# Optimization experiments

Hardware: AMD Instinct MI355X
Metric: run time of the kernel (lower is better)

The kernel has to match this reference:

```python
import jax, jax.numpy as jnp
import numpy as np

# ---- fixed problem dimensions ----
B, S, T = 64, 200, 32          # batch of sequences, trees per seq, nodes per tree
V, E, C = 50000, 128, 128      # vocab, embedding_dim, encode_dim
H, OUT = 100, 104              # GRU hidden, output_dim
N = B * S * T                  # total nodes
D_MAX = 5                      # max depth of a 32-node complete binary tree


def setup_inputs() -> dict:
    key = jax.random.key(0)
    ks = jax.random.split(key, 16)
    # --- tree structure: every tree is a complete binary tree with T nodes ---
    local_parent = np.array([0] + [(i - 1) // 2 for i in range(1, T)], dtype=np.int64)
    local_depth = np.array([int(np.floor(np.log2(i + 1))) for i in range(T)], dtype=np.int64)
    num_trees = B * S
    offsets = np.arange(num_trees, dtype=np.int64) * T
    node_parent = (offsets[:, None] + local_parent[None, :]).reshape(-1)
    node_depth = np.tile(local_depth, num_trees)
    node_tree = np.repeat(np.arange(num_trees, dtype=np.int64), T)
    node_tokens = jax.random.randint(ks[0], (N,), 0, V, dtype=jnp.int64)
    sc = 0.05
    inp = {
        "node_tokens": node_tokens,
        "node_parent": jnp.asarray(node_parent),
        "node_tree": jnp.asarray(node_tree),
        "node_depth": jnp.asarray(node_depth),
        "emb": jax.random.normal(ks[1], (V, E), jnp.float32) * sc,
        "w_lin": jax.random.normal(ks[2], (C, E), jnp.float32) * sc,
        "b_lin": jnp.zeros((C,), jnp.float32),
        "w_ih_f": jax.random.normal(ks[3], (3 * H, C), jnp.float32) * sc,
        "w_hh_f": jax.random.normal(ks[4], (3 * H, H), jnp.float32) * sc,
        "b_ih_f": jnp.zeros((3 * H,), jnp.float32),
        "b_hh_f": jnp.zeros((3 * H,), jnp.float32),
        "w_ih_b": jax.random.normal(ks[5], (3 * H, C), jnp.float32) * sc,
        "w_hh_b": jax.random.normal(ks[6], (3 * H, H), jnp.float32) * sc,
        "b_ih_b": jnp.zeros((3 * H,), jnp.float32),
        "b_hh_b": jnp.zeros((3 * H,), jnp.float32),
        "fc_w": jax.random.normal(ks[7], (OUT, 2 * H), jnp.float32) * sc,
        "fc_b": jnp.zeros((OUT,), jnp.float32),
    }
    return inp


def _gru(x_sbc, w_ih, w_hh, b_ih, b_hh):
    """Torch-convention GRU over leading time axis. x_sbc: [S, B, C] -> [S, B, H]."""
    h0 = jnp.zeros((x_sbc.shape[1], w_hh.shape[1]), x_sbc.dtype)

    def step(h, xt):
        gx = xt @ w_ih.T + b_ih
        gh = h @ w_hh.T + b_hh
        xr, xz, xn = jnp.split(gx, 3, axis=-1)
        hr, hz, hn = jnp.split(gh, 3, axis=-1)
        r = jax.nn.sigmoid(xr + hr)
        z = jax.nn.sigmoid(xz + hz)
        n = jnp.tanh(xn + r * hn)
        h_new = (1.0 - z) * n + z * h
        return h_new, h_new

    _, hs = jax.lax.scan(step, h0, x_sbc)
    return hs


def reference(node_tokens, node_parent, node_tree, node_depth,
              emb, w_lin, b_lin,
              w_ih_f, w_hh_f, b_ih_f, b_hh_f,
              w_ih_b, w_hh_b, b_ih_b, b_hh_b,
              fc_w, fc_b):
    # per-node contribution: W * emb(token) + b   (recursion base of hidden_state)
    c = emb[node_tokens] @ w_lin.T + b_lin               # [N, C]
    # level-batched bottom-up scatter-add: h(node) = c(node) + sum(h(children))
    h = c
    for d in range(D_MAX, 0, -1):
        mask = (node_depth == d)[:, None]
        h = h.at[node_parent].add(jnp.where(mask, h, 0.0))
    # per-tree max pool over all node hidden states (TreeEncoder output)
    tree_vec = jax.ops.segment_max(h, node_tree, num_segments=B * S)  # [B*S, C]
    x = tree_vec.reshape(B, S, C)
    # bidirectional GRU (batch_first in torch; scan over time here)
    x_t = jnp.transpose(x, (1, 0, 2))                    # [S, B, C]
    fwd = _gru(x_t, w_ih_f, w_hh_f, b_ih_f, b_hh_f)      # [S, B, H]
    bwd = _gru(x_t[::-1], w_ih_b, w_hh_b, b_ih_b, b_hh_b)[::-1]
    gru_out = jnp.concatenate([fwd, bwd], axis=-1)       # [S, B, 2H]
    pool = gru_out.max(axis=0)                           # [B, 2H] (max over time)
    return pool @ fc_w.T + fc_b                          # [B, OUT]
```

## Files before the change

kernel.cpp:

```cpp
#include <hip/hip_runtime.h>
#include <hip/hip_bf16.h>
#include <math.h>

#define BB 64
#define SS 200
#define TT 32
#define VV 50000
#define EE 128
#define CC 128
#define HH 100
#define G3 300
#define OUTD 104
#define NTREE (BB*SS)

typedef __attribute__((ext_vector_type(4))) float f32x4;
typedef _Float16 f16x8 __attribute__((ext_vector_type(8)));

#define L2E  1.4426950408889634f
#define NL2E (-1.4426950408889634f)
#define TL2E 2.8853900817779268f

#define BAR() asm volatile("s_waitcnt lgkmcnt(0)\n\ts_barrier" ::: "memory")


__global__ __launch_bounds__(256) void k0_prep(const float* __restrict__ w_lin,
                                               const float* __restrict__ w_ih_f,
                                               const float* __restrict__ w_ih_b,
                                               const float* __restrict__ emb,
                                               _Float16* __restrict__ wl,
                                               _Float16* __restrict__ k2b,
                                               _Float16* __restrict__ emb16) {
    const int tid  = threadIdx.x;
    const int wave = tid >> 6;
    const int lane = tid & 63;
    const int r = lane & 15;
    const int q = lane >> 4;
    if (blockIdx.x == 0) {
#pragma unroll
        for (int nt = 0; nt < 2; ++nt)
#pragma unroll
            for (int kt = 0; kt < 4; ++kt) {
                const int n = wave * 32 + nt * 16 + r;
                const float* src = w_lin + (long)n * EE + kt * 32 + q * 8;
                f16x8 f;
#pragma unroll
                for (int e = 0; e < 8; ++e) f[e] = (_Float16)src[e];
                *(f16x8*)&wl[(size_t)((((wave * 2 + nt) * 4 + kt) * 64) + lane) * 8] = f;
            }
    } else if (blockIdx.x <= 10) {
        const int nb = blockIdx.x - 1;
        const int n = nb * 64 + wave * 16 + r;
        const int dir = (n >= 320) ? 1 : 0;
        const int j = n - dir * 320;
        const int jj = (j < G3) ? j : 0;
        const float* w = dir ? w_ih_b : w_ih_f;
#pragma unroll
        for (int kt = 0; kt < 4; ++kt) {
            const float* src = w + (long)jj * EE + kt * 32 + q * 8;
            f16x8 f;
#pragma unroll
            for (int e = 0; e < 8; ++e) f[e] = (_Float16)src[e];
            *(f16x8*)&k2b[(size_t)((((nb * 4 + wave) * 4 + kt) * 64) + lane) * 8] = f;
        }
    } else {
        const long base = (long)(blockIdx.x - 11) * 2048 + (long)tid * 8;
        if (base < (long)VV * EE) {
            const float4* s = (const float4*)(emb + base);
            const float4 v0 = s[0], v1 = s[1];
            f16x8 f;
            f[0] = (_Float16)v0.x; f[1] = (_Float16)v0.y;
            f[2] = (_Float16)v0.z; f[3] = (_Float16)v0.w;
            f[4] = (_Float16)v1.x; f[5] = (_Float16)v1.y;
            f[6] = (_Float16)v1.z; f[7] = (_Float16)v1.w;
            *(f16x8*)&emb16[base] = f;
        }
    }
}

#define K1_TPI 2
#define AROWS (K1_TPI*TT)
#define LDA 136
#define LDC 132

__global__ __launch_bounds__(256) void k1_mfma(const int* __restrict__ tok,
                                               const _Float16* __restrict__ emb16,
                                               const _Float16* __restrict__ wl,
                                               const float* __restrict__ b_lin,
                                               _Float16* __restrict__ thi) {
    __shared__ __align__(16) _Float16 A_sh[AROWS * LDA];
    __shared__ __align__(16) float C_sh[AROWS * LDC];
    __shared__ int tok_sh[AROWS];

    const int tid  = threadIdx.x;
    const int wave = tid >> 6;
    const int lane = tid & 63;
    const int r = lane & 15;
    const int q = lane >> 4;

    f16x8 bfrag[2][4];
    float bias[2];
#pragma unroll
    for (int nt = 0; nt < 2; ++nt) {
        bias[nt] = b_lin[wave * 32 + nt * 16 + r];
#pragma unroll
        for (int kt = 0; kt < 4; ++kt)
            bfrag[nt][kt] = *(const f16x8*)&wl[(size_t)((((wave * 2 + nt) * 4 + kt) * 64) + lane) * 8];
    }

    const int tree0 = blockIdx.x * K1_TPI;
    if (tid < AROWS) tok_sh[tid] = tok[tree0 * TT + tid];
    __syncthreads();

#pragma unroll
    for (int i = 0; i < 4; ++i) {
        const int idx = tid + i * 256;
        const int row = idx >> 4;
        const int p   = idx & 15;
        const f16x8 v = *(const f16x8*)&emb16[(long)tok_sh[row] * EE + p * 8];
        *(f16x8*)&A_sh[row * LDA + p * 8] = v;
    }
    __syncthreads();

    f32x4 acc[4][2];
#pragma unroll
    for (int mt = 0; mt < 4; ++mt)
#pragma unroll
        for (int nt = 0; nt < 2; ++nt) acc[mt][nt] = (f32x4)(0.f);

#pragma unroll
    for (int mt = 0; mt < 4; ++mt) {
        const int m = mt * 16 + r;
        f16x8 afrag[4];
#pragma unroll
        for (int kt = 0; kt < 4; ++kt)
            afrag[kt] = *(const f16x8*)&A_sh[m * LDA + kt * 32 + q * 8];
#pragma unroll
        for (int nt = 0; nt < 2; ++nt)
#pragma unroll
            for (int kt = 0; kt < 4; ++kt)
                acc[mt][nt] = __builtin_amdgcn_mfma_f32_16x16x32_f16(
                    afrag[kt], bfrag[nt][kt], acc[mt][nt], 0, 0, 0);
    }

#pragma unroll
    for (int mt = 0; mt < 4; ++mt)
#pragma unroll
        for (int nt = 0; nt < 2; ++nt) {
            const int col = wave * 32 + nt * 16 + r;
#pragma unroll
            for (int reg = 0; reg < 4; ++reg) {
                const int row = mt * 16 + q * 4 + reg;
                C_sh[row * LDC + col] = acc[mt][nt][reg] + bias[nt];
            }
        }
    __syncthreads();

    {
        const int t = tid >> 7;
        const int j = tid & 127;
        const float* base = &C_sh[(t * TT) * LDC + j];
        float v[TT];
#pragma unroll
        for (int n = 0; n < TT; ++n) v[n] = base[n * LDC];
        float mx = -1e30f;
#pragma unroll
        for (int n = TT - 1; n >= 1; --n) {
            mx = fmaxf(mx, v[n]);
            v[(n - 1) >> 1] += v[n];
        }
        mx = fmaxf(mx, v[0]);
        thi[(size_t)(tree0 + t) * CC + j] = (_Float16)mx;
    }
}

__global__ __launch_bounds__(256) void k2_mfma(const _Float16* __restrict__ thi,
                                               const _Float16* __restrict__ k2b,
                                               const float* __restrict__ b_ih_f,
                                               const float* __restrict__ b_ih_b,
                                               const float* __restrict__ b_hh_f,
                                               const float* __restrict__ b_hh_b,
                                               float* __restrict__ gx) {
    __shared__ __align__(16) _Float16 Ah[32 * LDA];

    const int tid  = threadIdx.x;
    const int wave = tid >> 6;
    const int lane = tid & 63;
    const int r = lane & 15;
    const int q = lane >> 4;

    const int nb = blockIdx.x % 10;
    const int mb = blockIdx.x / 10;
    const int m0 = mb * 32;
    const int n0 = nb * 64;

#pragma unroll
    for (int i = 0; i < 2; ++i) {
        const int idx = tid + i * 256;
        const int row = idx >> 4;
        const int p   = idx & 15;
        f16x8 v = *(const f16x8*)&thi[(size_t)(m0 + row) * CC + p * 8];
        *(f16x8*)&Ah[row * LDA + p * 8] = v;
    }
    f16x8 bh[4];
#pragma unroll
    for (int kt = 0; kt < 4; ++kt)
        bh[kt] = *(const f16x8*)&k2b[(size_t)((((nb * 4 + wave) * 4 + kt) * 64) + lane) * 8];
    __syncthreads();

    f32x4 acc[2];
    acc[0] = (f32x4)(0.f); acc[1] = (f32x4)(0.f);
#pragma unroll
    for (int mt = 0; mt < 2; ++mt) {
        const int m = mt * 16 + r;
#pragma unroll
        for (int kt = 0; kt < 4; ++kt) {
            f16x8 a = *(const f16x8*)&Ah[m * LDA + kt * 32 + q * 8];
            acc[mt] = __builtin_amdgcn_mfma_f32_16x16x32_f16(a, bh[kt], acc[mt], 0, 0, 0);
        }
    }

    const int ng  = n0 + wave * 16 + r;
    const int dir = (ng >= 320) ? 1 : 0;
    const int j   = ng - dir * 320;
    const bool valid = (j < G3);
    const float* b_ih = dir ? b_ih_b : b_ih_f;
    const float* b_hh = dir ? b_hh_b : b_hh_f;
    const float bias = valid ? b_ih[j] : 0.f;
    const float bh2  = (valid && j < 2 * HH) ? b_hh[j] : 0.f;
    const float sc   = (j < 2 * HH) ? NL2E : TL2E;
    float* gxd = gx + (long)dir * NTREE * G3;
    if (valid) {
#pragma unroll
        for (int mt = 0; mt < 2; ++mt)
#pragma unroll
            for (int reg = 0; reg < 4; ++reg) {
                const int m = m0 + mt * 16 + q * 4 + reg;
                gxd[(long)m * G3 + j] = sc * (acc[mt][reg] + bias + bh2);
            }
    }
}

__global__ __launch_bounds__(256, 1) void k3_gru(const float* __restrict__ gx,
                                                 const float* __restrict__ w_hh_f,
                                                 const float* __restrict__ b_hh_f,
                                                 const float* __restrict__ w_hh_b,
                                                 const float* __restrict__ b_hh_b,
                                                 float* __restrict__ pool) {
    const int bid = blockIdx.x;
    const int dir = bid & 1;
    const int b = bid >> 1;
    const float* w_hh = dir ? w_hh_b : w_hh_f;
    const float* b_hh = dir ? b_hh_b : b_hh_f;

    __shared__ __align__(16) _Float16 h_sh[2][128];

    const int tid  = threadIdx.x;
    const int wave = tid >> 6;
    const int lane = tid & 63;
    const int r = lane & 15;
    const int q = lane >> 4;

    f16x8 bf[5][4];
#pragma unroll
    for (int i = 0; i < 5; ++i) {
        const int l = i * 16 + r;
        const int gate = l / 25;
        const int ch   = l - gate * 25;
        const bool nv  = (l < 75);
        const int row  = gate * HH + wave * 25 + ch;
        const float sc = (gate == 2) ? TL2E : NL2E;
#pragma unroll
        for (int kt = 0; kt < 4; ++kt) {
            f16x8 f;
#pragma unroll
            for (int e = 0; e < 8; ++e) {
                const int k = kt * 32 + q * 8 + e;
                f[e] = (_Float16)((nv && k < HH) ? sc * w_hh[row * HH + k] : 0.f);
            }
            bf[i][kt] = f;
        }
    }

    const int m = lane;
    const int c = wave * 25 + m;
    const bool act = (m < 25);
    const float bnc = act ? TL2E * b_hh[2 * HH + c] : 0.f;

    const int a_z  = (25 + m) & 63;
    const int a_n1 = (50 + m) & 63;
    const int a_n2 = (50 + m - 64) & 63;
    const bool nV1 = (50 + m) < 64;

    if (tid < 128) { h_sh[0][tid] = (_Float16)0.f; h_sh[1][tid] = (_Float16)0.f; }

    const int sstep = dir ? -1 : 1;
    const int s0 = dir ? (SS - 1) : 0;
    const float* gp = gx + (long)dir * NTREE * G3 + (long)b * SS * G3 + c;

    float pxr[4], pxz[4], pxn[4];
    if (act) {
#pragma unroll
        for (int j = 0; j < 4; ++j) {
            const long off = (long)(s0 + j * sstep) * G3;
            pxr[j] = gp[off]; pxz[j] = gp[off + HH]; pxn[j] = gp[off + 2 * HH];
        }
    }
    float hj = 0.f, hmax = -1e30f;
    __syncthreads();

    int s = s0;
    for (int t = 0; t < SS; t += 4) {
#pragma unroll
        for (int j = 0; j < 4; ++j) {
            const int p = j & 1;

            f16x8 a[4];
#pragma unroll
            for (int kt = 0; kt < 4; ++kt)
                a[kt] = *(const f16x8*)&h_sh[p][kt * 32 + q * 8];

            f32x4 accA[5], accB[5];
#pragma unroll
            for (int i = 0; i < 5; ++i) {
                accA[i] = (f32x4)(0.f);
                accB[i] = (f32x4)(0.f);
                accA[i] = __builtin_amdgcn_mfma_f32_16x16x32_f16(a[0], bf[i][0], accA[i], 0, 0, 0);
                accB[i] = __builtin_amdgcn_mfma_f32_16x16x32_f16(a[2], bf[i][2], accB[i], 0, 0, 0);
                accA[i] = __builtin_amdgcn_mfma_f32_16x16x32_f16(a[1], bf[i][1], accA[i], 0, 0, 0);
                accB[i] = __builtin_amdgcn_mfma_f32_16x16x32_f16(a[3], bf[i][3], accB[i], 0, 0, 0);
            }
            const float g0 = accA[0][0] + accB[0][0];
            const float g1 = accA[1][0] + accB[1][0];
            const float g2 = accA[2][0] + accB[2][0];
            const float g3 = accA[3][0] + accB[3][0];
            const float g4 = accA[4][0] + accB[4][0];
            float V1 = g0;
            V1 = (q == 1) ? g1 : V1;
            V1 = (q == 2) ? g2 : V1;
            V1 = (q == 3) ? g3 : V1;
            const float ghr = V1;
            const float ghz = __shfl(V1, a_z);
            const float vnA = __shfl(V1, a_n1);
            const float vnB = __shfl(g4, a_n2);
            const float ghn = nV1 ? vnA : vnB;

            if (act) {
                const float rg = __builtin_amdgcn_rcpf(1.f + __builtin_amdgcn_exp2f(pxr[j] + ghr));
                const float zg = __builtin_amdgcn_rcpf(1.f + __builtin_amdgcn_exp2f(pxz[j] + ghz));
                const float t1 = ghn + bnc;
                const float an = __builtin_fmaf(rg, t1, pxn[j]);
                const float u  = __builtin_amdgcn_rcpf(1.f + __builtin_amdgcn_exp2f(an));
                const float n  = __builtin_fmaf(-2.f, u, 1.f);
                hj = __builtin_fmaf(zg, hj - n, n);
                h_sh[1 - p][c] = (_Float16)hj;
                hmax = fmaxf(hmax, hj);
                if (t + j + 4 < SS) {
                    const long off = (long)(s + (j + 4) * sstep) * G3;
                    pxr[j] = gp[off]; pxz[j] = gp[off + HH]; pxn[j] = gp[off + 2 * HH];
                }
            }
            BAR();
        }
        s += 4 * sstep;
    }
    if (act) pool[(long)b * (2 * HH) + dir * HH + c] = hmax;
}

__global__ __launch_bounds__(256) void k4_fc(const float* __restrict__ pool,
                                             const float* __restrict__ fc_w,
                                             const float* __restrict__ fc_b,
                                             float* __restrict__ out) {
    const int b = blockIdx.x;
    __shared__ __align__(16) float p_sh[2 * HH];
    const int t = threadIdx.x;
    if (t < 2 * HH) p_sh[t] = pool[(long)b * (2 * HH) + t];
    __syncthreads();
    if (t < OUTD) {
        const float4* wr4 = (const float4*)(fc_w + (long)t * (2 * HH));
        const float4* p4 = (const float4*)p_sh;
        float a0 = 0.f, a1 = 0.f;
#pragma unroll
        for (int k = 0; k < 50; k += 2) {
            float4 w0 = wr4[k],   p0 = p4[k];
            float4 w1 = wr4[k+1], p1 = p4[k+1];
            a0 += w0.x*p0.x + w0.y*p0.y + w0.z*p0.z + w0.w*p0.w;
            a1 += w1.x*p1.x + w1.y*p1.y + w1.z*p1.z + w1.w*p1.w;
        }
        out[(long)b * OUTD + t] = fc_b[t] + a0 + a1;
    }
}

extern "C" void kernel_launch(void* const* d_in, const int* in_sizes, int n_in,
                              void* d_out, int out_size, void* d_ws, size_t ws_size,
                              hipStream_t stream) {
    const int*   tok    = (const int*)d_in[0];
    const float* emb    = (const float*)d_in[4];
    const float* w_lin  = (const float*)d_in[5];
    const float* b_lin  = (const float*)d_in[6];
    const float* w_ih_f = (const float*)d_in[7];
    const float* w_hh_f = (const float*)d_in[8];
    const float* b_ih_f = (const float*)d_in[9];
    const float* b_hh_f = (const float*)d_in[10];
    const float* w_ih_b = (const float*)d_in[11];
    const float* w_hh_b = (const float*)d_in[12];
    const float* b_ih_b = (const float*)d_in[13];
    const float* b_hh_b = (const float*)d_in[14];
    const float* fc_w   = (const float*)d_in[15];
    const float* fc_b   = (const float*)d_in[16];

    char* wsb = (char*)d_ws;
    _Float16* wl    = (_Float16*)(wsb);
    _Float16* k2b   = (_Float16*)(wsb + 32768);
    _Float16* thi   = (_Float16*)(wsb + 196608);
    float*    gx    = (float*)(wsb + 3473408);
    _Float16* emb16 = (_Float16*)(wsb + 3473408);
    float*    pool  = (float*)(wsb);
    float*    out   = (float*)d_out;

    k0_prep<<<11 + 3125, 256, 0, stream>>>(w_lin, w_ih_f, w_ih_b, emb, wl, k2b, emb16);
    k1_mfma<<<NTREE / K1_TPI, 256, 0, stream>>>(tok, emb16, wl, b_lin, thi);
    k2_mfma<<<(NTREE / 32) * 10, 256, 0, stream>>>(thi, k2b, b_ih_f, b_ih_b,
                                                   b_hh_f, b_hh_b, gx);
    k3_gru <<<2 * BB, 256, 0, stream>>>(gx, w_hh_f, b_hh_f, w_hh_b, b_hh_b, pool);
    k4_fc  <<<BB, 256, 0, stream>>>(pool, fc_w, fc_b, out);
}
```

Baseline: 232.0 us.

## Fuse embedding GEMM, tree reduce, and input-gate GEMM into one kernel

Drops the full fp32-to-fp16 conversion of the 50000x128 embedding table and instead gathers only the needed fp32 rows, converting them in-kernel. Merges the per-tree linear/tree-reduce kernel with the GRU input projection kernel, so each block processes 16 trees and keeps the pooled tree vectors in shared memory rather than round-tripping them through global memory. This removes a large conversion pass and one launch. In exchange, fp32 gathers double the bytes per gathered row, the grid has fewer, longer blocks with a serial loop, and there are extra barriers per chunk.

```diff
diff --git a/kernel.cpp b/kernel.cpp
--- a/kernel.cpp
+++ b/kernel.cpp
@@ -26,10 +26,8 @@
 __global__ __launch_bounds__(256) void k0_prep(const float* __restrict__ w_lin,
                                                const float* __restrict__ w_ih_f,
                                                const float* __restrict__ w_ih_b,
-                                               const float* __restrict__ emb,
                                                _Float16* __restrict__ wl,
-                                               _Float16* __restrict__ k2b,
-                                               _Float16* __restrict__ emb16) {
+                                               _Float16* __restrict__ k2b) {
     const int tid  = threadIdx.x;
     const int wave = tid >> 6;
     const int lane = tid & 63;
@@ -47,7 +45,7 @@
                 for (int e = 0; e < 8; ++e) f[e] = (_Float16)src[e];
                 *(f16x8*)&wl[(size_t)((((wave * 2 + nt) * 4 + kt) * 64) + lane) * 8] = f;
             }
-    } else if (blockIdx.x <= 10) {
+    } else {
         const int nb = blockIdx.x - 1;
         const int n = nb * 64 + wave * 16 + r;
         const int dir = (n >= 320) ? 1 : 0;
@@ -62,33 +60,28 @@
             for (int e = 0; e < 8; ++e) f[e] = (_Float16)src[e];
             *(f16x8*)&k2b[(size_t)((((nb * 4 + wave) * 4 + kt) * 64) + lane) * 8] = f;
         }
-    } else {
-        const long base = (long)(blockIdx.x - 11) * 2048 + (long)tid * 8;
-        if (base < (long)VV * EE) {
-            const float4* s = (const float4*)(emb + base);
-            const float4 v0 = s[0], v1 = s[1];
-            f16x8 f;
-            f[0] = (_Float16)v0.x; f[1] = (_Float16)v0.y;
-            f[2] = (_Float16)v0.z; f[3] = (_Float16)v0.w;
-            f[4] = (_Float16)v1.x; f[5] = (_Float16)v1.y;
-            f[6] = (_Float16)v1.z; f[7] = (_Float16)v1.w;
-            *(f16x8*)&emb16[base] = f;
-        }
-    }
-}
-
-#define K1_TPI 2
-#define AROWS (K1_TPI*TT)
+    }
+}
+
+#define TPB 16
+#define AROWS 64
 #define LDA 136
 #define LDC 132
 
-__global__ __launch_bounds__(256) void k1_mfma(const int* __restrict__ tok,
-                                               const _Float16* __restrict__ emb16,
-                                               const _Float16* __restrict__ wl,
-                                               const float* __restrict__ b_lin,
-                                               _Float16* __restrict__ thi) {
-    __shared__ __align__(16) _Float16 A_sh[AROWS * LDA];
-    __shared__ __align__(16) float C_sh[AROWS * LDC];
+__global__ __launch_bounds__(256, 4) void k12_fused(const int* __restrict__ tok,
+                                                    const float* __restrict__ emb,
+                                                    const _Float16* __restrict__ wl,
+                                                    const float* __restrict__ b_lin,
+                                                    const _Float16* __restrict__ k2b,
+                                                    const float* __restrict__ b_ih_f,
+                                                    const float* __restrict__ b_ih_b,
+                                                    const float* __restrict__ b_hh_f,
+                                                    const float* __restrict__ b_hh_b,
+                                                    float* __restrict__ gx) {
+    __shared__ __align__(16) char U_sh[AROWS * LDC * 4];
+    _Float16* A_sh = (_Float16*)U_sh;
+    float*    C_sh = (float*)U_sh;
+    __shared__ __align__(16) _Float16 thi_sh[TPB][LDA];
     __shared__ int tok_sh[AROWS];
 
     const int tid  = threadIdx.x;
@@ -97,6 +90,8 @@
     const int r = lane & 15;
     const int q = lane >> 4;
 
+    const int T0 = blockIdx.x * TPB;
+
     f16x8 bfrag[2][4];
     float bias[2];
 #pragma unroll
@@ -107,136 +102,109 @@
             bfrag[nt][kt] = *(const f16x8*)&wl[(size_t)((((wave * 2 + nt) * 4 + kt) * 64) + lane) * 8];
     }
 
-    const int tree0 = blockIdx.x * K1_TPI;
-    if (tid < AROWS) tok_sh[tid] = tok[tree0 * TT + tid];
+    for (int c = 0; c < 8; ++c) {
+        if (tid < AROWS) tok_sh[tid] = tok[(T0 + 2 * c) * TT + tid];
+        __syncthreads();
+
+#pragma unroll
+        for (int i = 0; i < 8; ++i) {
+            const int idx = tid + i * 256;
+            const int row = idx >> 5;
+            const int p   = idx & 31;
+            const float4 e = ((const float4*)(emb + (long)tok_sh[row] * EE))[p];
+            _Float16* dst = &A_sh[row * LDA + p * 4];
+            dst[0] = (_Float16)e.x; dst[1] = (_Float16)e.y;
+            dst[2] = (_Float16)e.z; dst[3] = (_Float16)e.w;
+        }
+        __syncthreads();
+
+        f32x4 acc[4][2];
+#pragma unroll
+        for (int mt = 0; mt < 4; ++mt)
+#pragma unroll
+            for (int nt = 0; nt < 2; ++nt) acc[mt][nt] = (f32x4)(0.f);
+
+#pragma unroll
+        for (int mt = 0; mt < 4; ++mt) {
+            const int m = mt * 16 + r;
+            f16x8 afrag[4];
+#pragma unroll
+            for (int kt = 0; kt < 4; ++kt)
+                afrag[kt] = *(const f16x8*)&A_sh[m * LDA + kt * 32 + q * 8];
+#pragma unroll
+            for (int nt = 0; nt < 2; ++nt)
+#pragma unroll
+                for (int kt = 0; kt < 4; ++kt)
+                    acc[mt][nt] = __builtin_amdgcn_mfma_f32_16x16x32_f16(
+                        afrag[kt], bfrag[nt][kt], acc[mt][nt], 0, 0, 0);
+        }
+        __syncthreads();
+
+#pragma unroll
+        for (int mt = 0; mt < 4; ++mt)
+#pragma unroll
+            for (int nt = 0; nt < 2; ++nt) {
+                const int col = wave * 32 + nt * 16 + r;
+#pragma unroll
+                for (int reg = 0; reg < 4; ++reg) {
+                    const int row = mt * 16 + q * 4 + reg;
+                    C_sh[row * LDC + col] = acc[mt][nt][reg] + bias[nt];
+                }
+            }
+        __syncthreads();
+
+        {
+            const int t = tid >> 7;
+            const int j = tid & 127;
+            const float* base = &C_sh[(t * TT) * LDC + j];
+            float v[TT];
+#pragma unroll
+            for (int n = 0; n < TT; ++n) v[n] = base[n * LDC];
+            float mx = -1e30f;
+#pragma unroll
+            for (int n = TT - 1; n >= 1; --n) {
+                mx = fmaxf(mx, v[n]);
+                v[(n - 1) >> 1] += v[n];
+            }
+            mx = fmaxf(mx, v[0]);
+            thi_sh[2 * c + t][j] = (_Float16)mx;
+        }
+    }
     __syncthreads();
 
-#pragma unroll
-    for (int i = 0; i < 4; ++i) {
-        const int idx = tid + i * 256;
-        const int row = idx >> 4;
-        const int p   = idx & 15;
-        const f16x8 v = *(const f16x8*)&emb16[(long)tok_sh[row] * EE + p * 8];
-        *(f16x8*)&A_sh[row * LDA + p * 8] = v;
-    }
-    __syncthreads();
-
-    f32x4 acc[4][2];
-#pragma unroll
-    for (int mt = 0; mt < 4; ++mt)
-#pragma unroll
-        for (int nt = 0; nt < 2; ++nt) acc[mt][nt] = (f32x4)(0.f);
-
-#pragma unroll
-    for (int mt = 0; mt < 4; ++mt) {
-        const int m = mt * 16 + r;
-        f16x8 afrag[4];
+    f16x8 a4[4];
+#pragma unroll
+    for (int kt = 0; kt < 4; ++kt)
+        a4[kt] = *(const f16x8*)&thi_sh[r][kt * 32 + q * 8];
+
+#pragma unroll
+    for (int nb = 0; nb < 10; ++nb) {
+        f16x8 bh[4];
 #pragma unroll
         for (int kt = 0; kt < 4; ++kt)
-            afrag[kt] = *(const f16x8*)&A_sh[m * LDA + kt * 32 + q * 8];
-#pragma unroll
-        for (int nt = 0; nt < 2; ++nt)
-#pragma unroll
-            for (int kt = 0; kt < 4; ++kt)
-                acc[mt][nt] = __builtin_amdgcn_mfma_f32_16x16x32_f16(
-                    afrag[kt], bfrag[nt][kt], acc[mt][nt], 0, 0, 0);
-    }
-
-#pragma unroll
-    for (int mt = 0; mt < 4; ++mt)
-#pragma unroll
-        for (int nt = 0; nt < 2; ++nt) {
-            const int col = wave * 32 + nt * 16 + r;
+            bh[kt] = *(const f16x8*)&k2b[(size_t)((((nb * 4 + wave) * 4 + kt) * 64) + lane) * 8];
+        f32x4 acc = (f32x4)(0.f);
+#pragma unroll
+        for (int kt = 0; kt < 4; ++kt)
+            acc = __builtin_amdgcn_mfma_f32_16x16x32_f16(a4[kt], bh[kt], acc, 0, 0, 0);
+
+        const int ng  = nb * 64 + wave * 16 + r;
+        const int dir = (ng >= 320) ? 1 : 0;
+        const int j   = ng - dir * 320;
+        const bool valid = (j < G3);
+        const float* b_ih = dir ? b_ih_b : b_ih_f;
+        const float* b_hh = dir ? b_hh_b : b_hh_f;
+        const float bias2 = valid ? b_ih[j] : 0.f;
+        const float bh2   = (valid && j < 2 * HH) ? b_hh[j] : 0.f;
+        const float sc    = (j < 2 * HH) ? NL2E : TL2E;
+        float* gxd = gx + (long)dir * NTREE * G3;
+        if (valid) {
 #pragma unroll
             for (int reg = 0; reg < 4; ++reg) {
-                const int row = mt * 16 + q * 4 + reg;
-                C_sh[row * LDC + col] = acc[mt][nt][reg] + bias[nt];
-            }
-        }
-    __syncthreads();
-
-    {
-        const int t = tid >> 7;
-        const int j = tid & 127;
-        const float* base = &C_sh[(t * TT) * LDC + j];
-        float v[TT];
-#pragma unroll
-        for (int n = 0; n < TT; ++n) v[n] = base[n * LDC];
-        float mx = -1e30f;
-#pragma unroll
-        for (int n = TT - 1; n >= 1; --n) {
-            mx = fmaxf(mx, v[n]);
-            v[(n - 1) >> 1] += v[n];
-        }
-        mx = fmaxf(mx, v[0]);
-        thi[(size_t)(tree0 + t) * CC + j] = (_Float16)mx;
-    }
-}
-
-__global__ __launch_bounds__(256) void k2_mfma(const _Float16* __restrict__ thi,
-                                               const _Float16* __restrict__ k2b,
-                                               const float* __restrict__ b_ih_f,
-                                               const float* __restrict__ b_ih_b,
-                                               const float* __restrict__ b_hh_f,
-                                               const float* __restrict__ b_hh_b,
-                                               float* __restrict__ gx) {
-    __shared__ __align__(16) _Float16 Ah[32 * LDA];
-
-    const int tid  = threadIdx.x;
-    const int wave = tid >> 6;
-    const int lane = tid & 63;
-    const int r = lane & 15;
-    const int q = lane >> 4;
-
-    const int nb = blockIdx.x % 10;
-    const int mb = blockIdx.x / 10;
-    const int m0 = mb * 32;
-    const int n0 = nb * 64;
-
-#pragma unroll
-    for (int i = 0; i < 2; ++i) {
-        const int idx = tid + i * 256;
-        const int row = idx >> 4;
-        const int p   = idx & 15;
-        f16x8 v = *(const f16x8*)&thi[(size_t)(m0 + row) * CC + p * 8];
-        *(f16x8*)&Ah[row * LDA + p * 8] = v;
-    }
-    f16x8 bh[4];
-#pragma unroll
-    for (int kt = 0; kt < 4; ++kt)
-        bh[kt] = *(const f16x8*)&k2b[(size_t)((((nb * 4 + wave) * 4 + kt) * 64) + lane) * 8];
-    __syncthreads();
-
-    f32x4 acc[2];
-    acc[0] = (f32x4)(0.f); acc[1] = (f32x4)(0.f);
-#pragma unroll
-    for (int mt = 0; mt < 2; ++mt) {
-        const int m = mt * 16 + r;
-#pragma unroll
-        for (int kt = 0; kt < 4; ++kt) {
-            f16x8 a = *(const f16x8*)&Ah[m * LDA + kt * 32 + q * 8];
-            acc[mt] = __builtin_amdgcn_mfma_f32_16x16x32_f16(a, bh[kt], acc[mt], 0, 0, 0);
-        }
-    }
-
-    const int ng  = n0 + wave * 16 + r;
-    const int dir = (ng >= 320) ? 1 : 0;
-    const int j   = ng - dir * 320;
-    const bool valid = (j < G3);
-    const float* b_ih = dir ? b_ih_b : b_ih_f;
-    const float* b_hh = dir ? b_hh_b : b_hh_f;
-    const float bias = valid ? b_ih[j] : 0.f;
-    const float bh2  = (valid && j < 2 * HH) ? b_hh[j] : 0.f;
-    const float sc   = (j < 2 * HH) ? NL2E : TL2E;
-    float* gxd = gx + (long)dir * NTREE * G3;
-    if (valid) {
-#pragma unroll
-        for (int mt = 0; mt < 2; ++mt)
-#pragma unroll
-            for (int reg = 0; reg < 4; ++reg) {
-                const int m = m0 + mt * 16 + q * 4 + reg;
-                gxd[(long)m * G3 + j] = sc * (acc[mt][reg] + bias + bh2);
-            }
+                const int m = T0 + q * 4 + reg;
+                gxd[(long)m * G3 + j] = sc * (acc[reg] + bias2 + bh2);
+            }
+        }
     }
 }
 
@@ -409,18 +377,15 @@
     const float* fc_b   = (const float*)d_in[16];
 
     char* wsb = (char*)d_ws;
-    _Float16* wl    = (_Float16*)(wsb);
-    _Float16* k2b   = (_Float16*)(wsb + 32768);
-    _Float16* thi   = (_Float16*)(wsb + 196608);
-    float*    gx    = (float*)(wsb + 3473408);
-    _Float16* emb16 = (_Float16*)(wsb + 3473408);
-    float*    pool  = (float*)(wsb);
-    float*    out   = (float*)d_out;
-
-    k0_prep<<<11 + 3125, 256, 0, stream>>>(w_lin, w_ih_f, w_ih_b, emb, wl, k2b, emb16);
-    k1_mfma<<<NTREE / K1_TPI, 256, 0, stream>>>(tok, emb16, wl, b_lin, thi);
-    k2_mfma<<<(NTREE / 32) * 10, 256, 0, stream>>>(thi, k2b, b_ih_f, b_ih_b,
-                                                   b_hh_f, b_hh_b, gx);
-    k3_gru <<<2 * BB, 256, 0, stream>>>(gx, w_hh_f, b_hh_f, w_hh_b, b_hh_b, pool);
-    k4_fc  <<<BB, 256, 0, stream>>>(pool, fc_w, fc_b, out);
-}
+    _Float16* wl   = (_Float16*)(wsb);
+    _Float16* k2b  = (_Float16*)(wsb + 32768);
+    float*    gx   = (float*)(wsb + 196608);
+    float*    pool = (float*)(wsb);
+    float*    out  = (float*)d_out;
+
+    k0_prep  <<<11, 256, 0, stream>>>(w_lin, w_ih_f, w_ih_b, wl, k2b);
+    k12_fused<<<NTREE / TPB, 256, 0, stream>>>(tok, emb, wl, b_lin, k2b,
+                                               b_ih_f, b_ih_b, b_hh_f, b_hh_b, gx);
+    k3_gru   <<<2 * BB, 256, 0, stream>>>(gx, w_hh_f, b_hh_f, w_hh_b, b_hh_b, pool);
+    k4_fc    <<<BB, 256, 0, stream>>>(pool, fc_w, fc_b, out);
+}
```

Result: no change. 230.4 us (-0.7%).
